# Performance work log

Measured on AMD Instinct MI355X. Metric: run time of the kernel, lower is better.

The kernel has to match this reference:

```python
import jax, jax.numpy as jnp
import numpy as np


def _schedule(epoch):
    # Mirrors SPLoss._adjust_N_ratio_q_t (epoch is a static Python int)
    if epoch <= 25:
        return 0.7, 2
    elif epoch <= 75:
        return 0.8, 0
    elif epoch <= 95:
        return 0.9, 0
    else:
        return 1.0, 0


def setup_inputs() -> dict:
    key = jax.random.key(0)
    k1, k2 = jax.random.split(key)
    B, C = 32768, 1000
    output = jax.random.normal(k1, (B, C), dtype=jnp.float32)
    target = jax.random.randint(k2, (B,), 0, C, dtype=jnp.int64)
    return {"output": output, "target": target, "epoch": 10}


def reference(output, target, epoch):
    N_ratio, q_t = _schedule(epoch)
    B = output.shape[0]
    # fused cross-entropy: log-softmax + per-sample gather
    logp = jax.nn.log_softmax(output, axis=-1)            # [B, C]
    ce_loss = -jnp.take_along_axis(logp, target[:, None], axis=1)[:, 0]  # [B]
    # sort-based quantile threshold
    sorted_ce = jnp.sort(ce_loss)                          # ascending
    lambda_t = sorted_ce[int(B * N_ratio)]
    # power reweight v_t = (1 - ce/lambda)^(1/(q_t-1)), zero past threshold, cap at 10
    exponent = 1.0 / (q_t - 1)
    v_t = (1.0 - ce_loss / lambda_t) ** exponent
    v_t = jnp.where(ce_loss >= lambda_t, 0.0, v_t)
    v_t = jnp.where(v_t >= 10.0, 10.0, v_t)
    return (ce_loss * v_t).mean()
```

## Files before the change

kernel.cpp:

```cpp
#include <hip/hip_runtime.h>
#include <math.h>


__device__ __forceinline__ unsigned f2u(float f) {
    unsigned u = __float_as_uint(f);
    return (u & 0x80000000u) ? ~u : (u | 0x80000000u);
}
__device__ __forceinline__ float u2f(unsigned u) {
    unsigned b = (u & 0x80000000u) ? (u & 0x7FFFFFFFu) : ~u;
    return __uint_as_float(b);
}

#define CE_WPB 4

__global__ __launch_bounds__(256) void ce_kernel(
        const float* __restrict__ x, const int* __restrict__ tgt,
        unsigned* __restrict__ ceu, unsigned* __restrict__ ghist, int B, int C)
{
    if (blockIdx.x == 0 && threadIdx.x < 256) ghist[threadIdx.x] = 0u;

    const int lane = threadIdx.x & 63;
    const int wave = threadIdx.x >> 6;
    const int row  = blockIdx.x * CE_WPB + wave;
    if (row >= B) return;

    const float* rp = x + (size_t)row * C;
    const int t = tgt[row];
    const float tv = rp[t];

    const int C4 = C >> 2;
    const float4* p4 = (const float4*)rp;
    const float NEG = -INFINITY;
    float4 v0 = make_float4(NEG, NEG, NEG, NEG), v1 = v0, v2 = v0, v3 = v0;
    if (lane       < C4) v0 = p4[lane];
    if (lane +  64 < C4) v1 = p4[lane + 64];
    if (lane + 128 < C4) v2 = p4[lane + 128];
    if (lane + 192 < C4) v3 = p4[lane + 192];

    float m = fmaxf(fmaxf(fmaxf(v0.x, v0.y), fmaxf(v0.z, v0.w)),
                    fmaxf(fmaxf(v1.x, v1.y), fmaxf(v1.z, v1.w)));
    m = fmaxf(m, fmaxf(fmaxf(v2.x, v2.y), fmaxf(v2.z, v2.w)));
    m = fmaxf(m, fmaxf(fmaxf(v3.x, v3.y), fmaxf(v3.z, v3.w)));
    for (int off = 32; off > 0; off >>= 1)
        m = fmaxf(m, __shfl_xor(m, off, 64));

    float s = __expf(v0.x - m) + __expf(v0.y - m) + __expf(v0.z - m) + __expf(v0.w - m)
            + __expf(v1.x - m) + __expf(v1.y - m) + __expf(v1.z - m) + __expf(v1.w - m)
            + __expf(v2.x - m) + __expf(v2.y - m) + __expf(v2.z - m) + __expf(v2.w - m)
            + __expf(v3.x - m) + __expf(v3.y - m) + __expf(v3.z - m) + __expf(v3.w - m);
    for (int off = 32; off > 0; off >>= 1)
        s += __shfl_xor(s, off, 64);

    if (lane == 0)
        ceu[row] = f2u((m + __logf(s)) - tv);
}

__global__ __launch_bounds__(512) void hist0_kernel(
        const unsigned* __restrict__ ceu, unsigned* __restrict__ ghist, int B)
{
    __shared__ unsigned wh[8][256];
    const int tid  = threadIdx.x;
    const int wave = tid >> 6;

    #pragma unroll
    for (int j = 0; j < 4; ++j) wh[(tid * 4 + j) >> 8][(tid * 4 + j) & 255] = 0u;
    __syncthreads();

    const int i = blockIdx.x * 512 + tid;
    if (i * 4 < B) {
        uint4 u = ((const uint4*)ceu)[i];
        atomicAdd(&wh[wave][u.x >> 24], 1u);
        atomicAdd(&wh[wave][u.y >> 24], 1u);
        atomicAdd(&wh[wave][u.z >> 24], 1u);
        atomicAdd(&wh[wave][u.w >> 24], 1u);
    }
    __syncthreads();

    if (tid < 256) {
        unsigned s = 0;
        #pragma unroll
        for (int w = 0; w < 8; ++w) s += wh[w][tid];
        if (s) atomicAdd(&ghist[tid], s);
    }
}

#define K2_T 1024
__global__ __launch_bounds__(K2_T) void select_kernel(
        const unsigned* __restrict__ ceu, const unsigned* __restrict__ ghist,
        const int* __restrict__ epoch_p, float* __restrict__ out, int B)
{
    __shared__ unsigned sv[32768];
    __shared__ unsigned sh[256];
    __shared__ unsigned s_prefix, s_k;
    __shared__ float    s_wsum[K2_T / 64];

    const int tid  = threadIdx.x;
    const int lane = tid & 63;
    const int wave = tid >> 6;

    const int n4 = B >> 2;
    for (int i = tid; i < n4; i += K2_T) ((uint4*)sv)[i] = ((const uint4*)ceu)[i];

    const int e = epoch_p[0];
    double nr; int qt;
    if (e <= 25)      { nr = 0.7; qt = 2; }
    else if (e <= 75) { nr = 0.8; qt = 0; }
    else if (e <= 95) { nr = 0.9; qt = 0; }
    else              { nr = 1.0; qt = 0; }
    const bool inv = (qt != 2);

    if (wave == 0) {
        long long kk = (long long)((double)B * nr);
        if (kk > (long long)B - 1) kk = (long long)B - 1;
        uint4 g = ((const uint4*)ghist)[lane];
        unsigned c0 = g.x, c1 = g.y, c2 = g.z, c3 = g.w;
        unsigned cw = c0 + c1 + c2 + c3;
        unsigned incl = cw;
        for (int off = 1; off < 64; off <<= 1) {
            unsigned t = __shfl_up(incl, off, 64);
            if (lane >= off) incl += t;
        }
        unsigned excl = incl - cw;
        unsigned kr = (unsigned)kk;
        unsigned long long bm = __ballot(excl <= kr && kr < excl + cw);
        int L = __ffsll(bm) - 1;
        if (lane == L) {
            unsigned rem = kr - excl;
            int b; unsigned cum;
            if      (rem < c0)           { b = 0; cum = 0; }
            else if (rem < c0 + c1)      { b = 1; cum = c0; }
            else if (rem < c0 + c1 + c2) { b = 2; cum = c0 + c1; }
            else                         { b = 3; cum = c0 + c1 + c2; }
            s_k = rem - cum;
            s_prefix = (unsigned)(4 * L + b) << 24;
        }
    }
    __syncthreads();

    for (int p = 1; p < 4; ++p) {
        if (tid < 256) sh[tid] = 0u;
        __syncthreads();
        const int shift = 24 - 8 * p;
        const unsigned hm   = 0xFFFFFFFFu << (shift + 8);
        const unsigned pref = s_prefix;
        for (int j = tid; j < B; j += K2_T) {
            unsigned u = sv[j];
            if ((u & hm) == (pref & hm))
                atomicAdd(&sh[(u >> shift) & 255u], 1u);
        }
        __syncthreads();
        if (wave == 0) {
            unsigned c0 = sh[4 * lane], c1 = sh[4 * lane + 1];
            unsigned c2 = sh[4 * lane + 2], c3 = sh[4 * lane + 3];
            unsigned cw = c0 + c1 + c2 + c3;
            unsigned incl = cw;
            for (int off = 1; off < 64; off <<= 1) {
                unsigned t = __shfl_up(incl, off, 64);
                if (lane >= off) incl += t;
            }
            unsigned excl = incl - cw;
            unsigned kr = s_k;
            unsigned long long bm = __ballot(excl <= kr && kr < excl + cw);
            int L = __ffsll(bm) - 1;
            if (lane == L) {
                unsigned rem = kr - excl;
                int b; unsigned cum;
                if      (rem < c0)           { b = 0; cum = 0; }
                else if (rem < c0 + c1)      { b = 1; cum = c0; }
                else if (rem < c0 + c1 + c2) { b = 2; cum = c0 + c1; }
                else                         { b = 3; cum = c0 + c1 + c2; }
                s_k = rem - cum;
                s_prefix = pref | ((unsigned)(4 * lane + b) << shift);
            }
        }
        __syncthreads();
    }

    const float lam = u2f(s_prefix);
    float part = 0.0f;
    for (int j = tid; j < B; j += K2_T) {
        float c = u2f(sv[j]);
        float base = 1.0f - c / lam;
        float v = inv ? (1.0f / base) : base;
        if (c >= lam)       v = 0.0f;
        else if (v >= 10.f) v = 10.0f;
        part += c * v;
    }
    for (int off = 32; off > 0; off >>= 1) part += __shfl_xor(part, off, 64);
    if (lane == 0) s_wsum[wave] = part;
    __syncthreads();
    if (tid == 0) {
        float tot = 0.0f;
        for (int i = 0; i < K2_T / 64; ++i) tot += s_wsum[i];
        out[0] = tot / (float)B;
    }
}

extern "C" void kernel_launch(void* const* d_in, const int* in_sizes, int n_in,
                              void* d_out, int out_size, void* d_ws, size_t ws_size,
                              hipStream_t stream)
{
    const float* x     = (const float*)d_in[0];
    const int*   tgt   = (const int*)d_in[1];
    const int*   epoch = (const int*)d_in[2];
    int B = in_sizes[1];
    int C = in_sizes[0] / B;

    unsigned* ceu   = (unsigned*)d_ws;
    unsigned* ghist = ceu + B;

    int ceBlocks = (B + CE_WPB - 1) / CE_WPB;
    ce_kernel<<<ceBlocks, 256, 0, stream>>>(x, tgt, ceu, ghist, B, C);
    hist0_kernel<<<16, 512, 0, stream>>>(ceu, ghist, B);
    select_kernel<<<1, K2_T, 0, stream>>>(ceu, ghist, epoch, (float*)d_out, B);
}
```

Measured before the change: 212.2 us.

## Fuse top-byte histogram into single-block select kernel with ballot-based aggregation

Drops the separate 16-block histogram kernel and the global histogram buffer. The single 1024-thread select block now builds the first-pass radix histogram while it copies ce values into shared memory. Instead of LDS atomics it uses a wave-level match loop (ballot, leader, popcount). This removes one kernel launch and the global atomics, but moves the first histogram pass onto a single CU and serialises the match loop per distinct byte value.

```diff
diff --git a/kernel.cpp b/kernel.cpp
--- a/kernel.cpp
+++ b/kernel.cpp
@@ -15,10 +15,8 @@
 
 __global__ __launch_bounds__(256) void ce_kernel(
         const float* __restrict__ x, const int* __restrict__ tgt,
-        unsigned* __restrict__ ceu, unsigned* __restrict__ ghist, int B, int C)
+        unsigned* __restrict__ ceu, int B, int C)
 {
-    if (blockIdx.x == 0 && threadIdx.x < 256) ghist[threadIdx.x] = 0u;
-
     const int lane = threadIdx.x & 63;
     const int wave = threadIdx.x >> 6;
     const int row  = blockIdx.x * CE_WPB + wave;
@@ -55,51 +53,60 @@
         ceu[row] = f2u((m + __logf(s)) - tv);
 }
 
-__global__ __launch_bounds__(512) void hist0_kernel(
-        const unsigned* __restrict__ ceu, unsigned* __restrict__ ghist, int B)
+#define K2_T 1024
+#define K2_W (K2_T / 64)
+
+__global__ __launch_bounds__(K2_T) void select_kernel(
+        const unsigned* __restrict__ ceu, const int* __restrict__ epoch_p,
+        float* __restrict__ out, int B)
 {
-    __shared__ unsigned wh[8][256];
+    __shared__ unsigned sv[32768];
+    __shared__ unsigned wh[K2_W][256];
+    __shared__ unsigned sh[256];
+    __shared__ unsigned s_prefix, s_k;
+    __shared__ float    s_wsum[K2_W];
+
     const int tid  = threadIdx.x;
+    const int lane = tid & 63;
     const int wave = tid >> 6;
 
     #pragma unroll
-    for (int j = 0; j < 4; ++j) wh[(tid * 4 + j) >> 8][(tid * 4 + j) & 255] = 0u;
-    __syncthreads();
-
-    const int i = blockIdx.x * 512 + tid;
-    if (i * 4 < B) {
-        uint4 u = ((const uint4*)ceu)[i];
-        atomicAdd(&wh[wave][u.x >> 24], 1u);
-        atomicAdd(&wh[wave][u.y >> 24], 1u);
-        atomicAdd(&wh[wave][u.z >> 24], 1u);
-        atomicAdd(&wh[wave][u.w >> 24], 1u);
+    for (int j = 0; j < 4; ++j) ((unsigned*)wh)[tid * 4 + j] = 0u;
+    __syncthreads();
+
+    const int n4    = B >> 2;
+    const int iters = (n4 + K2_T - 1) / K2_T;
+    for (int it = 0; it < iters; ++it) {
+        const int i = it * K2_T + tid;
+        const bool valid = (i < n4);
+        uint4 u = make_uint4(0u, 0u, 0u, 0u);
+        if (valid) { u = ((const uint4*)ceu)[i]; ((uint4*)sv)[i] = u; }
+        unsigned by[4] = { u.x >> 24, u.y >> 24, u.z >> 24, u.w >> 24 };
+        #pragma unroll
+        for (int c = 0; c < 4; ++c) {
+            bool done = !valid;
+            while (true) {
+                unsigned long long todo = __ballot(!done);
+                if (!todo) break;
+                int leader = (int)(__ffsll((long long)todo) - 1);
+                unsigned lb = __shfl(by[c], leader, 64);
+                bool match = (!done) && (by[c] == lb);
+                unsigned long long mm = __ballot(match);
+                if (lane == leader)
+                    wh[wave][lb] += (unsigned)__popcll(mm);
+                if (match) done = true;
+            }
+        }
     }
     __syncthreads();
 
     if (tid < 256) {
         unsigned s = 0;
         #pragma unroll
-        for (int w = 0; w < 8; ++w) s += wh[w][tid];
-        if (s) atomicAdd(&ghist[tid], s);
-    }
-}
-
-#define K2_T 1024
-__global__ __launch_bounds__(K2_T) void select_kernel(
-        const unsigned* __restrict__ ceu, const unsigned* __restrict__ ghist,
-        const int* __restrict__ epoch_p, float* __restrict__ out, int B)
-{
-    __shared__ unsigned sv[32768];
-    __shared__ unsigned sh[256];
-    __shared__ unsigned s_prefix, s_k;
-    __shared__ float    s_wsum[K2_T / 64];
-
-    const int tid  = threadIdx.x;
-    const int lane = tid & 63;
-    const int wave = tid >> 6;
-
-    const int n4 = B >> 2;
-    for (int i = tid; i < n4; i += K2_T) ((uint4*)sv)[i] = ((const uint4*)ceu)[i];
+        for (int w = 0; w < K2_W; ++w) s += wh[w][tid];
+        sh[tid] = s;
+    }
+    __syncthreads();
 
     const int e = epoch_p[0];
     double nr; int qt;
@@ -112,8 +119,8 @@
     if (wave == 0) {
         long long kk = (long long)((double)B * nr);
         if (kk > (long long)B - 1) kk = (long long)B - 1;
-        uint4 g = ((const uint4*)ghist)[lane];
-        unsigned c0 = g.x, c1 = g.y, c2 = g.z, c3 = g.w;
+        unsigned c0 = sh[4 * lane], c1 = sh[4 * lane + 1];
+        unsigned c2 = sh[4 * lane + 2], c3 = sh[4 * lane + 3];
         unsigned cw = c0 + c1 + c2 + c3;
         unsigned incl = cw;
         for (int off = 1; off < 64; off <<= 1) {
@@ -123,7 +130,7 @@
         unsigned excl = incl - cw;
         unsigned kr = (unsigned)kk;
         unsigned long long bm = __ballot(excl <= kr && kr < excl + cw);
-        int L = __ffsll(bm) - 1;
+        int L = (int)(__ffsll((long long)bm) - 1);
         if (lane == L) {
             unsigned rem = kr - excl;
             int b; unsigned cum;
@@ -161,7 +168,7 @@
             unsigned excl = incl - cw;
             unsigned kr = s_k;
             unsigned long long bm = __ballot(excl <= kr && kr < excl + cw);
-            int L = __ffsll(bm) - 1;
+            int L = (int)(__ffsll((long long)bm) - 1);
             if (lane == L) {
                 unsigned rem = kr - excl;
                 int b; unsigned cum;
@@ -191,7 +198,7 @@
     __syncthreads();
     if (tid == 0) {
         float tot = 0.0f;
-        for (int i = 0; i < K2_T / 64; ++i) tot += s_wsum[i];
+        for (int i = 0; i < K2_W; ++i) tot += s_wsum[i];
         out[0] = tot / (float)B;
     }
 }
@@ -206,11 +213,9 @@
     int B = in_sizes[1];
     int C = in_sizes[0] / B;
 
-    unsigned* ceu   = (unsigned*)d_ws;
-    unsigned* ghist = ceu + B;
+    unsigned* ceu = (unsigned*)d_ws;
 
     int ceBlocks = (B + CE_WPB - 1) / CE_WPB;
-    ce_kernel<<<ceBlocks, 256, 0, stream>>>(x, tgt, ceu, ghist, B, C);
-    hist0_kernel<<<16, 512, 0, stream>>>(ceu, ghist, B);
-    select_kernel<<<1, K2_T, 0, stream>>>(ceu, ghist, epoch, (float*)d_out, B);
-}
+    ce_kernel<<<ceBlocks, 256, 0, stream>>>(x, tgt, ceu, B, C);
+    select_kernel<<<1, K2_T, 0, stream>>>(ceu, epoch, (float*)d_out, B);
+}
```

After: 221.3 us. 1.04x slower.
